# Performance work log

Hardware: AMD Instinct MI355X
Metric: run time of the kernel (lower is better)

## Reference

```python
import jax, jax.numpy as jnp
import numpy as np
from jax import lax

NMS_RADIUS = 4
THRESHOLD = 0.005
BORDER = 4
MAX_KP = 1024


def _max_pool(x, r):
    # torch max_pool2d pads with -inf; reduce_window 'SAME' pads with init value.
    w = 2 * r + 1
    return lax.reduce_window(x, -jnp.inf, lax.max, (1, w, w), (1, 1, 1), 'SAME')


def simple_nms(scores, radius):
    zeros = jnp.zeros_like(scores)
    max_mask = scores == _max_pool(scores, radius)
    for _ in range(2):
        supp_mask = _max_pool(max_mask.astype(scores.dtype), radius) > 0
        supp_scores = jnp.where(supp_mask, zeros, scores)
        new_max_mask = supp_scores == _max_pool(supp_scores, radius)
        max_mask = max_mask | (new_max_mask & ~supp_mask)
    return jnp.where(max_mask, scores, zeros)


def sample_descriptors(kp, desc, s):
    """Bilinear grid_sample (align_corners=True, zero padding) + L2 normalize.
    kp: [B,N,2] (x,y) full-resolution pixel coords; desc: [B,C,h,w]."""
    b, c, h, w = desc.shape
    k = kp - s / 2 + 0.5
    gx = k[..., 0] / (w * s - 1) * 2.0 - 1.0
    gy = k[..., 1] / (h * s - 1) * 2.0 - 1.0
    x = (gx + 1.0) * 0.5 * (w - 1)  # align_corners=True mapping
    y = (gy + 1.0) * 0.5 * (h - 1)
    x0 = jnp.floor(x); y0 = jnp.floor(y)
    wx1 = x - x0; wy1 = y - y0
    x0i = x0.astype(jnp.int32); y0i = y0.astype(jnp.int32)

    def tap(d_b, xi, yi):  # d_b [C,h,w]; xi,yi [N] -> [C,N], zero outside
        v = ((xi >= 0) & (xi < w) & (yi >= 0) & (yi < h)).astype(d_b.dtype)
        g = d_b[:, jnp.clip(yi, 0, h - 1), jnp.clip(xi, 0, w - 1)]
        return g * v

    def one(d_b, x0i, y0i, wx1, wy1):
        wx0 = 1.0 - wx1; wy0 = 1.0 - wy1
        return (tap(d_b, x0i, y0i) * (wx0 * wy0)
                + tap(d_b, x0i + 1, y0i) * (wx1 * wy0)
                + tap(d_b, x0i, y0i + 1) * (wx0 * wy1)
                + tap(d_b, x0i + 1, y0i + 1) * (wx1 * wy1))

    out = jax.vmap(one)(desc, x0i, y0i, wx1, wy1)  # [B,C,N]
    n = jnp.maximum(jnp.linalg.norm(out, axis=1, keepdims=True), 1e-12)
    return out / n


def conv1x1(w, b, x):  # Conv1d kernel_size=1: [O,I] @ [B,I,N]
    return jnp.einsum('oi,bin->bon', w, x) + b[None, :, None]


def setup_inputs() -> dict:
    key = jax.random.key(0)
    ks = jax.random.split(key, 13)
    B, H, W = 4, 480, 640
    inp = {
        'scores': jax.random.uniform(ks[0], (B, H, W), jnp.float32),
        'd1': jax.random.normal(ks[1], (B, 64, H // 2, W // 2), jnp.float32),
        'd2': jax.random.normal(ks[2], (B, 128, H // 4, W // 4), jnp.float32),
        'cDa': jax.random.normal(ks[3], (B, 256, H // 8, W // 8), jnp.float32),
        'd4': jax.random.normal(ks[4], (B, 256, H // 16, W // 16), jnp.float32),
        'lin0_w': jax.random.normal(ks[5], (256, 256), jnp.float32) / np.sqrt(256),
        'lin0_b': jax.random.normal(ks[6], (256,), jnp.float32) * 0.01,
        'lin1_w': jax.random.normal(ks[7], (128, 128), jnp.float32) / np.sqrt(128),
        'lin1_b': jax.random.normal(ks[8], (128,), jnp.float32) * 0.01,
        'lin2_w': jax.random.normal(ks[9], (64, 64), jnp.float32) / np.sqrt(64),
        'lin2_b': jax.random.normal(ks[10], (64,), jnp.float32) * 0.01,
        'merge_w': jax.random.normal(ks[11], (256, 704), jnp.float32) / np.sqrt(704),
        'merge_b': jax.random.normal(ks[12], (256,), jnp.float32) * 0.01,
    }
    return inp


def reference(scores, d1, d2, cDa, d4, lin0_w, lin0_b, lin1_w, lin1_b,
              lin2_w, lin2_b, merge_w, merge_b):
    B, H, W = scores.shape
    s = simple_nms(scores, NMS_RADIUS)
    ys, xs = jnp.meshgrid(jnp.arange(H), jnp.arange(W), indexing='ij')
    valid = (ys >= BORDER) & (ys < H - BORDER) & (xs >= BORDER) & (xs < W - BORDER)
    masked = jnp.where(valid[None] & (s > THRESHOLD), s, -1.0)
    top_scores, idx = lax.top_k(masked.reshape(B, -1), MAX_KP)
    kx = (idx % W).astype(jnp.float32)
    ky = (idx // W).astype(jnp.float32)
    kp = jnp.stack([kx, ky], axis=-1)  # [B,K,2] (x,y), i.e. torch.flip(k,[1])
    de1 = sample_descriptors(kp, d1, 2)    # [B,64,K]
    de2 = sample_descriptors(kp, d2, 4)    # [B,128,K]
    de3 = sample_descriptors(kp, cDa, 8)   # [B,256,K]
    de4 = sample_descriptors(kp, d4, 16)   # [B,256,K]
    de4 = conv1x1(lin0_w, lin0_b, de4)
    de2 = conv1x1(lin1_w, lin1_b, de2)
    de1 = conv1x1(lin2_w, lin2_b, de1)
    descriptors = conv1x1(merge_w, merge_b,
                          jnp.concatenate([de1, de2, de3, de4], axis=1))
    return kp, top_scores, descriptors
```

## Files before the change

kernel.cpp:

```cpp
#include <hip/hip_runtime.h>
#include <hip/hip_bf16.h>

#define B 4
#define H 480
#define W 640
#define HW (H*W)
#define BHW (B*H*W)
#define NKP 1024
#define THRESH 0.005f
#define CAP 16384
#define NCOL (B*NKP)
#define KTOT 704

typedef __attribute__((ext_vector_type(8))) short s8v;
typedef __attribute__((ext_vector_type(4))) float f4v;
typedef struct { float x, y; } __attribute__((aligned(4))) f2u;

__device__ __forceinline__ short f2bf(float f) {
    __hip_bfloat16 h = __float2bfloat16(f);
    return *(short*)&h;
}

__device__ __forceinline__ float max3f(float a, float b, float c) {
    return fmaxf(fmaxf(a, b), c);
}
#define MAX9(A, base, str) \
    max3f(max3f((A)[(base)], (A)[(base)+(str)], (A)[(base)+2*(str)]), \
          max3f((A)[(base)+3*(str)], (A)[(base)+4*(str)], (A)[(base)+5*(str)]), \
          max3f((A)[(base)+6*(str)], (A)[(base)+7*(str)], (A)[(base)+8*(str)]))

__global__ __launch_bounds__(256) void fuse_w(const float* __restrict__ merge_w,
                                              const float* __restrict__ lin0_w,
                                              const float* __restrict__ lin1_w,
                                              const float* __restrict__ lin2_w,
                                              short* __restrict__ Mw) {
    __shared__ float red[4][64];
    int lane = threadIdx.x & 63;
    int wv = threadIdx.x >> 6;
    int jb = blockIdx.x;
    int o = blockIdx.y;
    int j = jb * 64 + lane;
    const float* mwr = merge_w + (size_t)o * KTOT;

    if (jb >= 3 && jb <= 6) {
        if (wv == 0) Mw[(size_t)o * KTOT + j] = f2bf(mwr[j]);
        return;
    }
    float acc = 0.0f;
    if (jb == 0) {
        int k0 = wv * 16;
        #pragma unroll
        for (int k = 0; k < 16; ++k)
            acc += mwr[k0 + k] * lin2_w[(k0 + k) * 64 + lane];
    } else if (jb <= 2) {
        int jj = (jb - 1) * 64 + lane;
        int k0 = wv * 32;
        #pragma unroll
        for (int k = 0; k < 32; ++k)
            acc += mwr[64 + k0 + k] * lin1_w[(k0 + k) * 128 + jj];
    } else {
        int jj = (jb - 7) * 64 + lane;
        int k0 = wv * 64;
        #pragma unroll
        for (int k = 0; k < 64; ++k)
            acc += mwr[448 + k0 + k] * lin0_w[(k0 + k) * 256 + jj];
    }
    red[wv][lane] = acc;
    __syncthreads();
    if (wv == 0) {
        float t = red[0][lane] + red[1][lane] + red[2][lane] + red[3][lane];
        Mw[(size_t)o * KTOT + j] = f2bf(t);
    }
}

__global__ __launch_bounds__(256) void fuse_bias(const float* __restrict__ merge_w,
                                                 const float* __restrict__ merge_b,
                                                 const float* __restrict__ lin0_b,
                                                 const float* __restrict__ lin1_b,
                                                 const float* __restrict__ lin2_b,
                                                 float* __restrict__ biasf,
                                                 int* __restrict__ cnt) {
    int lane = threadIdx.x & 63;
    int wv = threadIdx.x >> 6;
    int o = blockIdx.x * 4 + wv;
    if (blockIdx.x == 0 && threadIdx.x < 4) cnt[threadIdx.x * 64] = 0;
    const float* mwr = merge_w + (size_t)o * KTOT;
    float acc = 0.0f;
    #pragma unroll
    for (int i = 0; i < 11; ++i) {
        int k = i * 64 + lane;
        float c;
        if (k < 64) c = lin2_b[k];
        else if (k < 192) c = lin1_b[k - 64];
        else if (k < 448) c = 0.0f;
        else c = lin0_b[k - 448];
        acc += mwr[k] * c;
    }
    #pragma unroll
    for (int off = 32; off > 0; off >>= 1) acc += __shfl_xor(acc, off, 64);
    if (lane == 0) biasf[o] = merge_b[o] + acc;
}

__global__ __launch_bounds__(256) void transpose_d4(const float* __restrict__ d4,
                                                    float* __restrict__ d4T) {
    __shared__ float T[64][65];
    int b = blockIdx.z;
    int p0 = blockIdx.x * 64;
    int c0 = blockIdx.y * 64;
    for (int t = threadIdx.x; t < 4096; t += 256) {
        int ch = t >> 6, px = t & 63;
        int gp = p0 + px;
        if (gp < 1200)
            T[ch][px] = d4[((size_t)(b * 256 + c0 + ch)) * 1200 + gp];
    }
    __syncthreads();
    for (int t = threadIdx.x; t < 4096; t += 256) {
        int px = t >> 6, ch = t & 63;
        int gp = p0 + px;
        if (gp < 1200)
            d4T[((size_t)(b * 1200 + gp)) * 256 + c0 + ch] = T[ch][px];
    }
}

__global__ __launch_bounds__(256) void nms1(const float* __restrict__ scores,
                                            float* __restrict__ mask) {
    __shared__ float tile[40][40];
    __shared__ float hm[40][32];
    int bz = blockIdx.z;
    int x0 = blockIdx.x * 32, y0 = blockIdx.y * 32;
    const float* sp = scores + bz * HW;
    for (int t = threadIdx.x; t < 1600; t += 256) {
        int ly = t / 40, lx = t - ly * 40;
        int gy = y0 - 4 + ly, gx = x0 - 4 + lx;
        tile[ly][lx] = (gy >= 0 && gy < H && gx >= 0 && gx < W) ? sp[gy * W + gx] : -INFINITY;
    }
    __syncthreads();
    for (int t = threadIdx.x; t < 1280; t += 256) {
        int ly = t >> 5, lx = t & 31;
        hm[ly][lx] = MAX9(&tile[ly][0], lx, 1);
    }
    __syncthreads();
    for (int t = threadIdx.x; t < 1024; t += 256) {
        int ly = t >> 5, lx = t & 31;
        float m = MAX9(&hm[0][0], ly * 32 + lx, 32);
        float s = tile[ly + 4][lx + 4];
        mask[bz * HW + (y0 + ly) * W + x0 + lx] = (s == m) ? 1.0f : 0.0f;
    }
}

__global__ __launch_bounds__(512) void nms2_compact(const float* __restrict__ scores,
                                                    const float* __restrict__ mask0,
                                                    unsigned long long* __restrict__ cand,
                                                    int* __restrict__ cnt) {
    __shared__ float Sm[56 * 56];
    __shared__ float Mm[64 * 64];
    __shared__ float Zm[56 * 56];
    __shared__ float Tm[64 * 56];
    __shared__ int lcnt, gbase;
    int bz = blockIdx.z;
    int x0 = blockIdx.x * 32, y0 = blockIdx.y * 32;
    const float* sp = scores + bz * HW;
    const float* mp = mask0 + bz * HW;
    if (threadIdx.x == 0) lcnt = 0;
    for (int t = threadIdx.x; t < 4096; t += 512) {
        int ly = t >> 6, lx = t & 63;
        int gy = y0 - 16 + ly, gx = x0 - 16 + lx;
        Mm[t] = (gy >= 0 && gy < H && gx >= 0 && gx < W) ? mp[gy * W + gx] : 0.0f;
    }
    for (int t = threadIdx.x; t < 3136; t += 512) {
        int i = t / 56, j = t - i * 56;
        int gy = y0 - 12 + i, gx = x0 - 12 + j;
        Sm[t] = (gy >= 0 && gy < H && gx >= 0 && gx < W) ? sp[gy * W + gx] : -1.0f;
    }
    __syncthreads();
    for (int t = threadIdx.x; t < 3584; t += 512) {
        int i = t / 56, c = t - i * 56;
        Tm[i * 56 + c] = MAX9(Mm, i * 64 + c, 1);
    }
    __syncthreads();
    for (int t = threadIdx.x; t < 3136; t += 512) {
        int i = t / 56, c = t - i * 56;
        float m = MAX9(Tm, i * 56 + c, 56);
        Zm[t] = (m > 0.0f) ? -1.0f : Sm[t];
    }
    __syncthreads();
    for (int t = threadIdx.x; t < 2688; t += 512) {
        int i = t / 48, c = t - i * 48;
        Tm[i * 56 + c] = MAX9(Zm, i * 56 + c, 1);
    }
    __syncthreads();
    for (int t = threadIdx.x; t < 2304; t += 512) {
        int r = t / 48, c = t - r * 48;
        float m = MAX9(Tm, r * 56 + c, 56);
        float Zc = Zm[(r + 4) * 56 + c + 4];
        int mi = (r + 8) * 64 + c + 8;
        bool nm = (Zc == m) && (Zc >= 0.0f);
        Mm[mi] = (Mm[mi] != 0.0f || nm) ? 1.0f : 0.0f;
    }
    __syncthreads();
    for (int t = threadIdx.x; t < 1920; t += 512) {
        int r = t / 40, c = t - r * 40;
        Tm[r * 56 + c] = MAX9(Mm, (r + 8) * 64 + c + 8, 1);
    }
    __syncthreads();
    for (int t = threadIdx.x; t < 1600; t += 512) {
        int r = t / 40, c = t - r * 40;
        float m = MAX9(Tm, r * 56 + c, 56);
        int zi = (r + 8) * 56 + c + 8;
        Zm[zi] = (m > 0.0f) ? -1.0f : Sm[zi];
    }
    __syncthreads();
    for (int t = threadIdx.x; t < 1280; t += 512) {
        int r = t / 32, c = t & 31;
        Tm[r * 56 + c] = MAX9(Zm, (r + 8) * 56 + c + 8, 1);
    }
    __syncthreads();
    unsigned long long keys[2];
    int nl = 0;
    #pragma unroll
    for (int q = 0; q < 2; ++q) {
        int t = threadIdx.x + q * 512;
        int r3 = t >> 5, c = t & 31;
        float m = MAX9(Tm, r3 * 56 + c, 56);
        float Zc = Zm[(r3 + 12) * 56 + c + 12];
        bool fin = (Mm[(r3 + 16) * 64 + c + 16] != 0.0f) || ((Zc == m) && (Zc >= 0.0f));
        int gy = y0 + r3, gx = x0 + c;
        float sc = Sm[(r3 + 12) * 56 + c + 12];
        if (fin && gy >= 4 && gy < H - 4 && gx >= 4 && gx < W - 4 && sc > THRESH) {
            unsigned r = (unsigned)(gy * W + gx);
            unsigned bits = __float_as_uint(sc) | 0x80000000u;
            keys[nl++] = ((unsigned long long)bits << 32) |
                         (unsigned long long)(0xFFFFFFFFu - r);
        }
    }
    int lpos = 0;
    if (nl) lpos = atomicAdd(&lcnt, nl);
    __syncthreads();
    if (threadIdx.x == 0) gbase = (lcnt > 0) ? atomicAdd(&cnt[bz * 64], lcnt) : 0;
    __syncthreads();
    for (int j = 0; j < nl; ++j) {
        int p = gbase + lpos + j;
        if (p < CAP) cand[(size_t)bz * CAP + p] = keys[j];
    }
}

__global__ __launch_bounds__(1024) void topk(const unsigned long long* __restrict__ cand,
                                             const int* __restrict__ cnt,
                                             float* __restrict__ out, int* __restrict__ fidx,
                                             int* __restrict__ perm) {
    __shared__ int hist[2048];
    __shared__ unsigned long long buf[4096];
    __shared__ int scnt, spiv1, spiv2, sabove;
    int b = blockIdx.x, tid = threadIdx.x;
    int m = cnt[b * 64]; if (m > CAP) m = CAP;
    const unsigned long long* cb = cand + (size_t)b * CAP;
    int target = (m < 1024) ? m : 1024;

    hist[tid] = 0; hist[tid + 1024] = 0;
    if (tid == 0) { scnt = 0; spiv1 = 2048; spiv2 = 0; sabove = 0; }
    __syncthreads();
    for (int i = tid; i < m; i += 1024)
        atomicAdd(&hist[(int)(cb[i] >> 53) & 0x7FF], 1);
    __syncthreads();
    for (int d = 1; d < 2048; d <<= 1) {
        int v0 = hist[tid] + ((tid + d < 2048) ? hist[tid + d] : 0);
        int v1 = hist[tid + 1024] + ((tid + 1024 + d < 2048) ? hist[tid + 1024 + d] : 0);
        __syncthreads();
        hist[tid] = v0; hist[tid + 1024] = v1;
        __syncthreads();
    }
    if (target > 0) {
        for (int t = tid; t < 2048; t += 1024) {
            int c = hist[t];
            int cn = (t < 2047) ? hist[t + 1] : 0;
            if (c >= target && cn < target) { spiv1 = t; sabove = cn; }
        }
    }
    __syncthreads();
    int piv1 = spiv1;
    int target2 = target - sabove;
    hist[tid] = 0; hist[tid + 1024] = 0;
    __syncthreads();
    for (int i = tid; i < m; i += 1024) {
        unsigned long long k = cb[i];
        if (((int)(k >> 53) & 0x7FF) == piv1)
            atomicAdd(&hist[(int)(k >> 42) & 0x7FF], 1);
    }
    __syncthreads();
    for (int d = 1; d < 2048; d <<= 1) {
        int v0 = hist[tid] + ((tid + d < 2048) ? hist[tid + d] : 0);
        int v1 = hist[tid + 1024] + ((tid + 1024 + d < 2048) ? hist[tid + 1024 + d] : 0);
        __syncthreads();
        hist[tid] = v0; hist[tid + 1024] = v1;
        __syncthreads();
    }
    if (target > 0) {
        for (int t = tid; t < 2048; t += 1024) {
            int c = hist[t];
            int cn = (t < 2047) ? hist[t + 1] : 0;
            if (c >= target2 && cn < target2) spiv2 = t;
        }
    }
    __syncthreads();
    int piv2 = spiv2;
    for (int i = tid; i < m; i += 1024) {
        unsigned long long k = cb[i];
        int b1 = (int)(k >> 53) & 0x7FF;
        bool sel = (target > 0) &&
                   (b1 > piv1 || (b1 == piv1 && (((int)(k >> 42) & 0x7FF) >= piv2)));
        if (sel) {
            int p = atomicAdd(&scnt, 1);
            if (p < 4096) buf[p] = k;
        }
    }
    __syncthreads();
    int sc_ = scnt; if (sc_ > 4096) sc_ = 4096;
    int ns = 1024; while (ns < sc_) ns <<= 1;
    for (int t = tid; t < ns; t += 1024) if (t >= sc_) buf[t] = 0ULL;
    __syncthreads();
    for (int k = 2; k <= ns; k <<= 1)
        for (int j = k >> 1; j > 0; j >>= 1) {
            __syncthreads();
            for (int t = tid; t < ns; t += 1024) {
                int ixj = t ^ j;
                if (ixj > t) {
                    unsigned long long a = buf[t], bb = buf[ixj];
                    if (((t & k) == 0) ? (a < bb) : (a > bb)) { buf[t] = bb; buf[ixj] = a; }
                }
            }
        }
    __syncthreads();
    unsigned long long key = buf[tid];
    float kx, ky, sc;
    unsigned idx;
    if (key != 0ULL) {
        unsigned ord = (unsigned)(key >> 32);
        sc = __uint_as_float(ord ^ 0x80000000u);
        idx = 0xFFFFFFFFu - (unsigned)(key & 0xFFFFFFFFu);
        kx = (float)(idx % W);
        ky = (float)(idx / W);
    } else {
        sc = -1.0f; idx = 0; kx = 0.0f; ky = 0.0f;
    }
    int bn = b * NKP + tid;
    out[bn * 2 + 0] = kx;
    out[bn * 2 + 1] = ky;
    out[B * NKP * 2 + bn] = sc;
    fidx[bn] = (int)idx;
    __syncthreads();
    if (tid < 512) { hist[tid] = 0; hist[tid + 1024] = 0; }
    __syncthreads();
    int bucket = (int)(idx >> 10);
    atomicAdd(&hist[bucket], 1);
    __syncthreads();
    if (tid < 512) hist[512 + tid] = hist[tid];
    __syncthreads();
    for (int d = 1; d < 512; d <<= 1) {
        int v = 0;
        if (tid < 512) v = hist[512 + tid] + ((tid >= d) ? hist[512 + tid - d] : 0);
        __syncthreads();
        if (tid < 512) hist[512 + tid] = v;
        __syncthreads();
    }
    int intra = atomicAdd(&hist[1024 + bucket], 1);
    int pos = hist[512 + bucket] - hist[bucket] + intra;
    perm[b * NKP + pos] = tid;
}

__global__ __launch_bounds__(256) void sample_all(const float* __restrict__ d1,
                                                  const float* __restrict__ d2,
                                                  const float* __restrict__ cDa,
                                                  const float* __restrict__ d4T,
                                                  const int* __restrict__ fidx,
                                                  const int* __restrict__ perm,
                                                  short* __restrict__ X) {
    int lane = threadIdx.x & 63;
    int wv = threadIdx.x >> 6;
    int seg = blockIdx.y;
    int bid = blockIdx.x;
    int swz = ((bid & 7) << 7) | (bid >> 3);
    int b = swz >> 8;
    int g0 = ((swz & 255) << 2) + wv;

    const float* map; int h, w, s, C, base, nset;
    if (seg == 0)      { map = d1;  h = 240; w = 320; s = 2;  C = 64;  base = 0;   nset = 1; }
    else if (seg == 1) { map = d2;  h = 120; w = 160; s = 4;  C = 128; base = 64;  nset = 2; }
    else if (seg == 2) { map = cDa; h = 60;  w = 80;  s = 8;  C = 256; base = 192; nset = 4; }
    else               { map = d4T; h = 30;  w = 40;  s = 16; C = 256; base = 448; nset = 4; }

    int col = (b << 10) | perm[(b << 10) + g0];
    int idx = fidx[col];
    float kx = (float)(idx % W);
    float ky = (float)(idx / W);
    float kxs = kx - (float)s * 0.5f + 0.5f;
    float kys = ky - (float)s * 0.5f + 0.5f;
    float gx = kxs / (float)(w * s - 1) * 2.0f - 1.0f;
    float gy = kys / (float)(h * s - 1) * 2.0f - 1.0f;
    float x = (gx + 1.0f) * 0.5f * (float)(w - 1);
    float y = (gy + 1.0f) * 0.5f * (float)(h - 1);
    float x0f = floorf(x), y0f = floorf(y);
    int x0 = (int)x0f, y0 = (int)y0f;
    float wx1 = x - x0f, wy1 = y - y0f;
    float wx0 = 1.0f - wx1, wy0 = 1.0f - wy1;
    bool vx0 = (x0 >= 0) && (x0 < w);
    bool vx1 = (x0 + 1 >= 0) && (x0 + 1 < w);
    bool vy0 = (y0 >= 0) && (y0 < h);
    bool vy1 = (y0 + 1 >= 0) && (y0 + 1 < h);
    int xc0 = min(max(x0, 0), w - 1), xc1 = min(max(x0 + 1, 0), w - 1);
    int yc0 = min(max(y0, 0), h - 1), yc1 = min(max(y0 + 1, 0), h - 1);
    float w00 = (vx0 && vy0) ? wx0 * wy0 : 0.0f;
    float w01 = (vx1 && vy0) ? wx1 * wy0 : 0.0f;
    float w10 = (vx0 && vy1) ? wx0 * wy1 : 0.0f;
    float w11 = (vx1 && vy1) ? wx1 * wy1 : 0.0f;

    float vals[4];
    float r = 0.0f;
    if (seg == 3) {
        const float* pt = d4T + ((size_t)b * 1200) * 256 + lane;
        size_t o00 = ((size_t)(yc0 * 40 + xc0)) << 8;
        size_t o01 = ((size_t)(yc0 * 40 + xc1)) << 8;
        size_t o10 = ((size_t)(yc1 * 40 + xc0)) << 8;
        size_t o11 = ((size_t)(yc1 * 40 + xc1)) << 8;
        float q00[4], q01[4], q10[4], q11[4];
        #pragma unroll
        for (int j = 0; j < 4; ++j) {
            q00[j] = pt[o00 + j * 64]; q01[j] = pt[o01 + j * 64];
            q10[j] = pt[o10 + j * 64]; q11[j] = pt[o11 + j * 64];
        }
        #pragma unroll
        for (int j = 0; j < 4; ++j) {
            vals[j] = q00[j] * w00 + q01[j] * w01 + q10[j] * w10 + q11[j] * w11;
            r += vals[j] * vals[j];
        }
    } else {
        int xb = min(xc0, w - 2);
        float s0 = (xc0 == xb) ? 1.0f : 0.0f;
        float s1 = (xc1 == xb) ? 1.0f : 0.0f;
        float ax = w00 * s0 + w01 * s1;
        float ay = w00 * (1.0f - s0) + w01 * (1.0f - s1);
        float bx = w10 * s0 + w11 * s1;
        float by = w10 * (1.0f - s0) + w11 * (1.0f - s1);
        size_t hw = (size_t)(h * w);
        const float* pb = map + ((size_t)b * C + lane) * hw;
        size_t off0 = (size_t)yc0 * w + xb;
        size_t off1 = (size_t)yc1 * w + xb;
        size_t cstr = hw << 6;
        f2u q0[4], q1[4];
        #pragma unroll
        for (int j = 0; j < 4; ++j) {
            if (j < nset) {
                const float* p = pb + (size_t)j * cstr;
                q0[j] = *(const f2u*)(p + off0);
                q1[j] = *(const f2u*)(p + off1);
            }
        }
        #pragma unroll
        for (int j = 0; j < 4; ++j) {
            if (j < nset) {
                vals[j] = q0[j].x * ax + q0[j].y * ay + q1[j].x * bx + q1[j].y * by;
                r += vals[j] * vals[j];
            }
        }
    }
    #pragma unroll
    for (int off = 32; off > 0; off >>= 1) r += __shfl_xor(r, off, 64);
    float denom = fmaxf(sqrtf(r), 1e-12f);
    float inv = 1.0f / denom;
    short* xp = X + (size_t)col * KTOT + base + lane;
    #pragma unroll
    for (int j = 0; j < 4; ++j) {
        if (j < nset) xp[j * 64] = f2bf(vals[j] * inv);
    }
}

__global__ __launch_bounds__(256) void gemm_mfma(const short* __restrict__ Mw,
                                                 const short* __restrict__ X,
                                                 const float* __restrict__ biasf,
                                                 float* __restrict__ out) {
    __shared__ short As[64 * 72];
    __shared__ short Bs[64 * 72];
    int tid = threadIdx.x;
    int lane = tid & 63, w = tid >> 6;
    int r = lane & 15, quad = lane >> 4;
    int rowBase = blockIdx.y * 64, colBase = blockIdx.x * 64;
    int sm = tid >> 2, skq = (tid & 3) << 4;

    const short* pa = Mw + (size_t)(rowBase + sm) * KTOT + skq;
    const short* pb = X + (size_t)(colBase + sm) * KTOT + skq;
    s8v a0 = *(const s8v*)(pa), a1 = *(const s8v*)(pa + 8);
    s8v b0 = *(const s8v*)(pb), b1 = *(const s8v*)(pb + 8);

    f4v acc[4];
    #pragma unroll
    for (int t = 0; t < 4; ++t) acc[t] = (f4v)0.0f;

    for (int kt = 0; kt < 11; ++kt) {
        __syncthreads();
        *(s8v*)&As[sm * 72 + skq + 0] = a0;
        *(s8v*)&As[sm * 72 + skq + 8] = a1;
        *(s8v*)&Bs[sm * 72 + skq + 0] = b0;
        *(s8v*)&Bs[sm * 72 + skq + 8] = b1;
        __syncthreads();
        if (kt < 10) {
            pa += 64; pb += 64;
            a0 = *(const s8v*)(pa); a1 = *(const s8v*)(pa + 8);
            b0 = *(const s8v*)(pb); b1 = *(const s8v*)(pb + 8);
        }
        #pragma unroll
        for (int kk = 0; kk < 2; ++kk) {
            int aoff = (w * 16 + r) * 72 + kk * 32 + quad * 8;
            s8v af = *(const s8v*)&As[aoff];
            #pragma unroll
            for (int t = 0; t < 4; ++t) {
                int boff = (t * 16 + r) * 72 + kk * 32 + quad * 8;
                s8v bf = *(const s8v*)&Bs[boff];
                acc[t] = __builtin_amdgcn_mfma_f32_16x16x32_bf16(af, bf, acc[t], 0, 0, 0);
            }
        }
    }
    #pragma unroll
    for (int t = 0; t < 4; ++t) {
        int colg = colBase + t * 16 + r;
        size_t obase = (size_t)(colg >> 10) * (256 * NKP) + (size_t)(colg & 1023);
        #pragma unroll
        for (int reg = 0; reg < 4; ++reg) {
            int row = rowBase + w * 16 + quad * 4 + reg;
            out[obase + (size_t)row * NKP] = acc[t][reg] + biasf[row];
        }
    }
}

extern "C" void kernel_launch(void* const* d_in, const int* in_sizes, int n_in,
                              void* d_out, int out_size, void* d_ws, size_t ws_size,
                              hipStream_t stream) {
    const float* scores  = (const float*)d_in[0];
    const float* d1      = (const float*)d_in[1];
    const float* d2      = (const float*)d_in[2];
    const float* cDa     = (const float*)d_in[3];
    const float* d4      = (const float*)d_in[4];
    const float* lin0_w  = (const float*)d_in[5];
    const float* lin0_b  = (const float*)d_in[6];
    const float* lin1_w  = (const float*)d_in[7];
    const float* lin1_b  = (const float*)d_in[8];
    const float* lin2_w  = (const float*)d_in[9];
    const float* lin2_b  = (const float*)d_in[10];
    const float* merge_w = (const float*)d_in[11];
    const float* merge_b = (const float*)d_in[12];
    float* out = (float*)d_out;

    char* ws = (char*)d_ws;
    float* MASK = (float*)ws;
    short* Xbuf = (short*)ws;
    float* d4T  = (float*)(ws + 6291456);
    unsigned long long* cand  = (unsigned long long*)(ws + 14745600);
    int* cnt                  = (int*)(ws + 15269888);
    int* fidx                 = (int*)(ws + 15401984);
    short* Mw                 = (short*)(ws + 15418368);
    float* biasf              = (float*)(ws + 16139264);
    int* perm                 = (int*)(ws + 16140288);

    dim3 tgrid(W / 32, H / 32, B);

    fuse_w<<<dim3(11, 256), 256, 0, stream>>>(merge_w, lin0_w, lin1_w, lin2_w, Mw);
    fuse_bias<<<64, 256, 0, stream>>>(merge_w, merge_b, lin0_b, lin1_b, lin2_b, biasf, cnt);
    transpose_d4<<<dim3(19, 4, 4), 256, 0, stream>>>(d4, d4T);
    nms1<<<tgrid, 256, 0, stream>>>(scores, MASK);
    nms2_compact<<<tgrid, 512, 0, stream>>>(scores, MASK, cand, cnt);
    topk<<<B, 1024, 0, stream>>>(cand, cnt, out, fidx, perm);
    sample_all<<<dim3(1024, 4), 256, 0, stream>>>(d1, d2, cDa, d4T, fidx, perm, Xbuf);
    gemm_mfma<<<dim3(NCOL / 64, 256 / 64), 256, 0, stream>>>(Mw, Xbuf, biasf, out + B * NKP * 3);
}
```

Baseline: 312.2 us.

## Fuse first NMS max-pool pass into the compaction kernel with larger halo

Merges the separate nms1 kernel, which wrote a full float mask to global memory, into the nms2_compact kernel. The fused kernel loads a 72x72 score tile (20-pixel halo) and recomputes the initial max mask for the 64x64 region in shared memory, so the global mask round-trip and one kernel launch go away. In exchange each block loads a bigger halo, does redundant max-pool work on overlapping borders, and uses more shared memory, which may lower occupancy.

Measured after the change: 310.2 us. About the same (-0.7%).

```diff
diff --git a/kernel.cpp b/kernel.cpp
--- a/kernel.cpp
+++ b/kernel.cpp
@@ -122,66 +122,47 @@
     }
 }
 
-__global__ __launch_bounds__(256) void nms1(const float* __restrict__ scores,
-                                            float* __restrict__ mask) {
-    __shared__ float tile[40][40];
-    __shared__ float hm[40][32];
-    int bz = blockIdx.z;
-    int x0 = blockIdx.x * 32, y0 = blockIdx.y * 32;
-    const float* sp = scores + bz * HW;
-    for (int t = threadIdx.x; t < 1600; t += 256) {
-        int ly = t / 40, lx = t - ly * 40;
-        int gy = y0 - 4 + ly, gx = x0 - 4 + lx;
-        tile[ly][lx] = (gy >= 0 && gy < H && gx >= 0 && gx < W) ? sp[gy * W + gx] : -INFINITY;
-    }
-    __syncthreads();
-    for (int t = threadIdx.x; t < 1280; t += 256) {
-        int ly = t >> 5, lx = t & 31;
-        hm[ly][lx] = MAX9(&tile[ly][0], lx, 1);
-    }
-    __syncthreads();
-    for (int t = threadIdx.x; t < 1024; t += 256) {
-        int ly = t >> 5, lx = t & 31;
-        float m = MAX9(&hm[0][0], ly * 32 + lx, 32);
-        float s = tile[ly + 4][lx + 4];
-        mask[bz * HW + (y0 + ly) * W + x0 + lx] = (s == m) ? 1.0f : 0.0f;
-    }
-}
-
-__global__ __launch_bounds__(512) void nms2_compact(const float* __restrict__ scores,
-                                                    const float* __restrict__ mask0,
-                                                    unsigned long long* __restrict__ cand,
-                                                    int* __restrict__ cnt) {
-    __shared__ float Sm[56 * 56];
+__global__ __launch_bounds__(512) void nms_fused(const float* __restrict__ scores,
+                                                 unsigned long long* __restrict__ cand,
+                                                 int* __restrict__ cnt) {
+    __shared__ float S72[72 * 72];
+    __shared__ float T72[72 * 64];
     __shared__ float Mm[64 * 64];
     __shared__ float Zm[56 * 56];
-    __shared__ float Tm[64 * 56];
     __shared__ int lcnt, gbase;
     int bz = blockIdx.z;
     int x0 = blockIdx.x * 32, y0 = blockIdx.y * 32;
     const float* sp = scores + bz * HW;
-    const float* mp = mask0 + bz * HW;
     if (threadIdx.x == 0) lcnt = 0;
+    for (int t = threadIdx.x; t < 5184; t += 512) {
+        int i = t / 72, j = t - i * 72;
+        int gy = y0 - 20 + i, gx = x0 - 20 + j;
+        S72[t] = (gy >= 0 && gy < H && gx >= 0 && gx < W) ? sp[gy * W + gx] : -1.0f;
+    }
+    __syncthreads();
+    for (int t = threadIdx.x; t < 4608; t += 512) {
+        int i = t >> 6, c = t & 63;
+        T72[i * 64 + c] = MAX9(S72, i * 72 + c, 1);
+    }
+    __syncthreads();
     for (int t = threadIdx.x; t < 4096; t += 512) {
-        int ly = t >> 6, lx = t & 63;
-        int gy = y0 - 16 + ly, gx = x0 - 16 + lx;
-        Mm[t] = (gy >= 0 && gy < H && gx >= 0 && gx < W) ? mp[gy * W + gx] : 0.0f;
-    }
-    for (int t = threadIdx.x; t < 3136; t += 512) {
-        int i = t / 56, j = t - i * 56;
-        int gy = y0 - 12 + i, gx = x0 - 12 + j;
-        Sm[t] = (gy >= 0 && gy < H && gx >= 0 && gx < W) ? sp[gy * W + gx] : -1.0f;
-    }
-    __syncthreads();
+        int r = t >> 6, c = t & 63;
+        float m = MAX9(T72, r * 64 + c, 64);
+        float s = S72[(r + 4) * 72 + c + 4];
+        int gy = y0 - 16 + r, gx = x0 - 16 + c;
+        Mm[t] = (gy >= 0 && gy < H && gx >= 0 && gx < W && s == m) ? 1.0f : 0.0f;
+    }
+    __syncthreads();
+    float* Tm = T72;
     for (int t = threadIdx.x; t < 3584; t += 512) {
         int i = t / 56, c = t - i * 56;
         Tm[i * 56 + c] = MAX9(Mm, i * 64 + c, 1);
     }
     __syncthreads();
     for (int t = threadIdx.x; t < 3136; t += 512) {
-        int i = t / 56, c = t - i * 56;
-        float m = MAX9(Tm, i * 56 + c, 56);
-        Zm[t] = (m > 0.0f) ? -1.0f : Sm[t];
+        int i = t / 56, j = t - i * 56;
+        float m = MAX9(Tm, i * 56 + j, 56);
+        Zm[t] = (m > 0.0f) ? -1.0f : S72[(i + 8) * 72 + (j + 8)];
     }
     __syncthreads();
     for (int t = threadIdx.x; t < 2688; t += 512) {
@@ -207,7 +188,7 @@
         int r = t / 40, c = t - r * 40;
         float m = MAX9(Tm, r * 56 + c, 56);
         int zi = (r + 8) * 56 + c + 8;
-        Zm[zi] = (m > 0.0f) ? -1.0f : Sm[zi];
+        Zm[zi] = (m > 0.0f) ? -1.0f : S72[(r + 16) * 72 + (c + 16)];
     }
     __syncthreads();
     for (int t = threadIdx.x; t < 1280; t += 512) {
@@ -225,7 +206,7 @@
         float Zc = Zm[(r3 + 12) * 56 + c + 12];
         bool fin = (Mm[(r3 + 16) * 64 + c + 16] != 0.0f) || ((Zc == m) && (Zc >= 0.0f));
         int gy = y0 + r3, gx = x0 + c;
-        float sc = Sm[(r3 + 12) * 56 + c + 12];
+        float sc = S72[(r3 + 20) * 72 + (c + 20)];
         if (fin && gy >= 4 && gy < H - 4 && gx >= 4 && gx < W - 4 && sc > THRESH) {
             unsigned r = (unsigned)(gy * W + gx);
             unsigned bits = __float_as_uint(sc) | 0x80000000u;
@@ -549,7 +530,6 @@
     float* out = (float*)d_out;
 
     char* ws = (char*)d_ws;
-    float* MASK = (float*)ws;
     short* Xbuf = (short*)ws;
     float* d4T  = (float*)(ws + 6291456);
     unsigned long long* cand  = (unsigned long long*)(ws + 14745600);
@@ -564,8 +544,7 @@
     fuse_w<<<dim3(11, 256), 256, 0, stream>>>(merge_w, lin0_w, lin1_w, lin2_w, Mw);
     fuse_bias<<<64, 256, 0, stream>>>(merge_w, merge_b, lin0_b, lin1_b, lin2_b, biasf, cnt);
     transpose_d4<<<dim3(19, 4, 4), 256, 0, stream>>>(d4, d4T);
-    nms1<<<tgrid, 256, 0, stream>>>(scores, MASK);
-    nms2_compact<<<tgrid, 512, 0, stream>>>(scores, MASK, cand, cnt);
+    nms_fused<<<tgrid, 512, 0, stream>>>(scores, cand, cnt);
     topk<<<B, 1024, 0, stream>>>(cand, cnt, out, fidx, perm);
     sample_all<<<dim3(1024, 4), 256, 0, stream>>>(d1, d2, cDa, d4T, fidx, perm, Xbuf);
     gemm_mfma<<<dim3(NCOL / 64, 256 / 64), 256, 0, stream>>>(Mw, Xbuf, biasf, out + B * NKP * 3);
```
